# Kernel tuning notes

Measured on AMD Instinct MI355X. Metric: run time of the kernel, lower is better.

## Reference

```python
import jax, jax.numpy as jnp
import numpy as np

N_QUBITS = 6
N_LAYERS = 2
QSVT_DEGREE = 3
DT_RANK = max(N_QUBITS // 2, 1)
OUT_DIM = 3 * N_QUBITS
PI = np.float32(np.pi)
DT_MIN, DT_MAX = 1e-3, 0.1
BATCH, SEQ = 256, 512


def _ry_mat(theta):
    c = jnp.cos(theta / 2)
    s = jnp.sin(theta / 2)
    row0 = jnp.stack([c, -s], axis=-1)
    row1 = jnp.stack([s, c], axis=-1)
    return jnp.stack([row0, row1], axis=-2).astype(jnp.complex64)


def _rz_mat(theta):
    e = jnp.exp(-0.5j * theta.astype(jnp.complex64))
    z = jnp.zeros_like(e)
    row0 = jnp.stack([e, z], axis=-1)
    row1 = jnp.stack([z, jnp.conj(e)], axis=-1)
    return jnp.stack([row0, row1], axis=-2)


def _rx_mat(theta):
    c = jnp.cos(theta / 2).astype(jnp.complex64)
    s = jnp.sin(theta / 2).astype(jnp.complex64)
    row0 = jnp.stack([c, -1j * s], axis=-1)
    row1 = jnp.stack([-1j * s, c], axis=-1)
    return jnp.stack([row0, row1], axis=-2)


def _apply1(state, mat, w):
    # state: (B, 2, ..., 2) tensor over N_QUBITS axes; mat: (2,2) or batched (B,2,2)
    state = jnp.moveaxis(state, 1 + w, -1)
    if mat.ndim == 3:
        state = jnp.einsum('bij,b...j->b...i', mat, state)
    else:
        state = jnp.einsum('ij,b...j->b...i', mat, state)
    return jnp.moveaxis(state, -1, 1 + w)


def _cnot(state, c, t):
    state = jnp.moveaxis(state, (1 + c, 1 + t), (-2, -1))
    state = state.at[..., 1, :].set(state[..., 1, ::-1])
    return jnp.moveaxis(state, (-2, -1), (1 + c, 1 + t))


def _crx(state, theta, c, t):
    state = jnp.moveaxis(state, (1 + c, 1 + t), (-2, -1))
    m = _rx_mat(theta)
    state = state.at[..., 1, :].set(jnp.einsum('ij,...j->...i', m, state[..., 1, :]))
    return jnp.moveaxis(state, (-2, -1), (1 + c, 1 + t))


def _circuit(h, x, dt, circuit_params, poly_coeffs, qsvt_params):
    """Batched statevector simulation of the selective QSVT + unified ansatz qnode."""
    n = N_QUBITS
    B = h.shape[0]
    state = jnp.zeros((B,) + (2,) * n, jnp.complex64)
    state = state.at[(slice(None),) + (0,) * n].set(1.0 + 0.0j)
    # 1) state encoding RY(h[t-1])
    for i in range(n):
        state = _apply1(state, _ry_mat(h[:, i]), i)
    # 2) Delta-modulated QSVT: RZ rotations + bidirectional CNOT ring per degree
    qidx = 0
    n_qp = n * QSVT_DEGREE
    for deg in range(QSVT_DEGREE + 1):
        coeff = poly_coeffs[deg]
        for i in range(n):
            if qidx < n_qp:
                ang = coeff * dt[:, i] * qsvt_params[qidx] * PI
                qidx += 1
            else:
                ang = coeff * dt[:, i] * PI
            state = _apply1(state, _rz_mat(ang), i)
        for i in range(n - 1):
            state = _cnot(state, i, i + 1)
        state = _cnot(state, n - 1, 0)
        for i in range(n - 1, 0, -1):
            state = _cnot(state, i, i - 1)
    # 3) unified variational ansatz
    p = 0
    for _ in range(N_LAYERS):
        for i in range(n):
            state = _apply1(state, _rx_mat(circuit_params[p]), i)
            state = _apply1(state, _ry_mat(circuit_params[p + 1]), i)
            state = _apply1(state, _rz_mat(circuit_params[p + 2]), i)
            p += 3
        for i in range(n):
            state = _crx(state, circuit_params[p], i, (i + 1) % n)
            p += 1
        for i in range(n - 1, -1, -1):
            state = _crx(state, circuit_params[p], i, (i - 1) % n)
            p += 1
    # 4) Delta-modulated input RY(x * dt)
    for i in range(n):
        state = _apply1(state, _ry_mat(x[:, i] * dt[:, i]), i)
    # 5) Pauli X/Y/Z expectation values per qubit
    xs, ys, zs = [], [], []
    for i in range(n):
        s = jnp.moveaxis(state, 1 + i, 1).reshape(B, 2, -1)
        z = jnp.sum(jnp.conj(s[:, 0]) * s[:, 1], axis=-1)
        xs.append(2.0 * jnp.real(z))
        ys.append(2.0 * jnp.imag(z))
        zs.append(jnp.sum(jnp.abs(s[:, 0]) ** 2 - jnp.abs(s[:, 1]) ** 2, axis=-1))
    return jnp.stack(xs + ys + zs, axis=-1).astype(jnp.float32)  # (B, 3n)


def setup_inputs() -> dict:
    key = jax.random.key(0)
    ks = jax.random.split(key, 8)
    angles = jax.random.uniform(ks[0], (BATCH, SEQ, N_QUBITS), jnp.float32) * PI
    Wx = jax.random.normal(ks[1], (DT_RANK + 2 * N_QUBITS, N_QUBITS), jnp.float32) / np.float32(np.sqrt(N_QUBITS))
    Wdt = jax.random.normal(ks[2], (N_QUBITS, DT_RANK), jnp.float32) / np.float32(np.sqrt(DT_RANK))
    dt = jnp.exp(jax.random.uniform(ks[3], (N_QUBITS,), jnp.float32) * np.float32(np.log(DT_MAX) - np.log(DT_MIN)) + np.float32(np.log(DT_MIN)))
    bdt = dt + jnp.log(-jnp.expm1(-dt))
    poly_coeffs = jax.random.normal(ks[4], (QSVT_DEGREE + 1,), jnp.float32) * 0.1
    qsvt_params = jax.random.normal(ks[5], (N_QUBITS * QSVT_DEGREE,), jnp.float32) * 0.1
    circuit_params = jax.random.normal(ks[6], (5 * N_QUBITS * N_LAYERS,), jnp.float32) * 0.1
    D = jnp.ones((OUT_DIM,), jnp.float32)
    Wc = jax.random.normal(ks[7], (OUT_DIM, N_QUBITS), jnp.float32) / np.float32(np.sqrt(N_QUBITS))
    return {"angles": angles, "Wx": Wx, "Wdt": Wdt, "bdt": bdt, "poly_coeffs": poly_coeffs, "qsvt_params": qsvt_params, "circuit_params": circuit_params, "D": D, "Wc": Wc}


def reference(angles, Wx, Wdt, bdt, poly_coeffs, qsvt_params, circuit_params, D, Wc):
    x_dbc = angles @ Wx.T  # (B,S, dt_rank + 2n)
    dt_raw = x_dbc[..., :DT_RANK]
    # B slice computed in the original but never used in forward
    C = x_dbc[..., DT_RANK + N_QUBITS:]
    dt_angles = jnp.tanh(jax.nn.softplus(dt_raw @ Wdt.T + bdt)) * PI  # (B,S,n)
    # quantum part is detached in the original (detach().cpu() before the qnode)
    sg = jax.lax.stop_gradient
    xs = (jnp.moveaxis(sg(angles), 1, 0), jnp.moveaxis(sg(dt_angles), 1, 0))
    cp, pc, qp = sg(circuit_params), sg(poly_coeffs), sg(qsvt_params)
    h0 = jnp.zeros((angles.shape[0], N_QUBITS), jnp.float32)

    def step(h, xt):
        x_t, dt_t = xt
        meas = _circuit(h, x_t, dt_t, cp, pc, qp)
        return meas[:, 2 * N_QUBITS:], meas  # carry = PauliZ block

    _, meas = jax.lax.scan(step, h0, xs)
    h_full = jnp.moveaxis(meas, 0, 1)  # (B,S,3n)
    return (C @ Wc.T) * h_full + D * jnp.concatenate([angles] * 3, axis=-1)
```

## Files before the change

### kernel.cpp

```cpp
#include <hip/hip_runtime.h>
#include <math.h>

#define BATCH 256
#define SEQ 512
#define SDS 54
#define PI_F 3.14159265358979323846f

template<int CTRL>
__device__ __forceinline__ float fdpp(float v) {
    return __int_as_float(__builtin_amdgcn_mov_dpp(__float_as_int(v), CTRL, 0xF, 0xF, true));
}
template<int L>
__device__ __forceinline__ float rdl(float v) {
    return __int_as_float(__builtin_amdgcn_readlane(__float_as_int(v), L));
}
__device__ __forceinline__ float rdlv(float v, int l) {
    return __int_as_float(__builtin_amdgcn_readlane(__float_as_int(v), l));
}
template<int M>
__device__ __forceinline__ float shxm(float v) {
    if constexpr (M == 1)       return fdpp<0xB1>(v);
    else if constexpr (M == 2)  return fdpp<0x4E>(v);
    else if constexpr (M == 8)  return fdpp<0x128>(v);
    else if constexpr (M == 32) return __shfl_xor(v, 32, 64);
    else return __int_as_float(__builtin_amdgcn_ds_swizzle(__float_as_int(v), (M << 10) | 0x1F));
}
__device__ __forceinline__ float redsum64(float v) {
    v += fdpp<0x128>(v);
    v += fdpp<0x124>(v);
    v += fdpp<0x122>(v);
    v += fdpp<0x121>(v);
    return (rdl<0>(v) + rdl<16>(v)) + (rdl<32>(v) + rdl<48>(v));
}
__device__ __forceinline__ float xorf(float v, int m) {
    return __int_as_float(__float_as_int(v) ^ m);
}
__device__ __forceinline__ int permf(int x) {
    const int cs[11] = {0,1,2,3,4,5,5,4,3,2,1};
    const int ts[11] = {1,2,3,4,5,0,4,3,2,1,0};
#pragma unroll
    for (int k = 10; k >= 0; k--) {
        int cb = (x >> (5 - cs[k])) & 1;
        x ^= cb << (5 - ts[k]);
    }
    return x;
}
__device__ __forceinline__ void cmul4(const float* c,
    float vr, float vi, float ar, float ai, float br, float bi, float cr, float ci,
    float& nr, float& ni) {
    nr = c[0]*vr - c[1]*vi + c[2]*ar - c[3]*ai + c[4]*br - c[5]*bi + c[6]*cr - c[7]*ci;
    ni = c[0]*vi + c[1]*vr + c[2]*ai + c[3]*ar + c[4]*bi + c[5]*br + c[6]*ci + c[7]*cr;
}
__device__ __forceinline__ void ringapply(const float* rc,
    float vr, float vi, float br, float bi, float cr, float ci, float dr, float di,
    float& nr, float& ni) {
    nr = rc[0]*vr - rc[1]*bi - rc[2]*ci + rc[3]*dr;
    ni = rc[0]*vi + rc[1]*br + rc[2]*cr + rc[3]*di;
}

__global__ __launch_bounds__(256) void prep_kernel(
    const float* __restrict__ angles, const float* __restrict__ Wx,
    const float* __restrict__ Wdt, const float* __restrict__ bdt,
    const float* __restrict__ D, const float* __restrict__ Wc,
    float* __restrict__ sd)
{
    int gid = blockIdx.x * blockDim.x + threadIdx.x;
    if (gid >= BATCH * SEQ) return;
    const float* a = angles + (size_t)gid * 6;
    float ang[6];
#pragma unroll
    for (int i = 0; i < 6; i++) ang[i] = a[i];
    float dtr[3];
#pragma unroll
    for (int r = 0; r < 3; r++) {
        float s = 0.f;
#pragma unroll
        for (int k = 0; k < 6; k++) s += ang[k] * Wx[r * 6 + k];
        dtr[r] = s;
    }
    float* rec = sd + (size_t)gid * SDS;
    float dtv[6];
#pragma unroll
    for (int i = 0; i < 6; i++) {
        float x = bdt[i];
#pragma unroll
        for (int r = 0; r < 3; r++) x += dtr[r] * Wdt[i * 3 + r];
        float sp = (x > 15.f) ? x : log1pf(expf(x));
        dtv[i] = tanhf(sp) * PI_F;
        rec[i] = dtv[i];
        float th = ang[i] * dtv[i];
        rec[6 + i]  = cosf(th);
        rec[12 + i] = sinf(th);
    }
    float C[6];
#pragma unroll
    for (int i = 0; i < 6; i++) {
        float s = 0.f;
#pragma unroll
        for (int k = 0; k < 6; k++) s += ang[k] * Wx[(9 + i) * 6 + k];
        C[i] = s;
    }
#pragma unroll
    for (int j = 0; j < 18; j++) {
        float s = 0.f;
#pragma unroll
        for (int i = 0; i < 6; i++) s += C[i] * Wc[j * 6 + i];
        rec[18 + j] = s;
        rec[36 + j] = D[j] * ang[j % 6];
    }
}

__global__ __launch_bounds__(64) void umat_kernel(const float* __restrict__ cp,
                                                  float2* __restrict__ um)
{
    const int lane = threadIdx.x;
    const int col = blockIdx.x;
    int bitv[6];
#pragma unroll
    for (int i = 0; i < 6; i++) bitv[i] = (lane >> (5 - i)) & 1;

    float qc[2][3][8], rc[2][6][4];
#pragma unroll
    for (int l = 0; l < 2; l++) {
        float g00r[6], g00i[6], g01r[6], g01i[6], g10r[6], g10i[6], g11r[6], g11i[6];
#pragma unroll
        for (int i = 0; i < 6; i++) {
            float ax = cp[l * 30 + i * 3 + 0];
            float ay = cp[l * 30 + i * 3 + 1];
            float az = cp[l * 30 + i * 3 + 2];
            float ca = cosf(0.5f * ax), sa = sinf(0.5f * ax);
            float cb = cosf(0.5f * ay), sb = sinf(0.5f * ay);
            float cg = cosf(0.5f * az), sg = sinf(0.5f * az);
            float m00r = cb * ca, m00i =  sb * sa;
            float m01r = -sb * ca, m01i = -cb * sa;
            float m10r =  sb * ca, m10i = -cb * sa;
            float m11r =  cb * ca, m11i = -sb * sa;
            g00r[i] = cg * m00r + sg * m00i; g00i[i] = cg * m00i - sg * m00r;
            g01r[i] = cg * m01r + sg * m01i; g01i[i] = cg * m01i - sg * m01r;
            g10r[i] = cg * m10r - sg * m10i; g10i[i] = cg * m10i + sg * m10r;
            g11r[i] = cg * m11r - sg * m11i; g11i[i] = cg * m11i + sg * m11r;
        }
#pragma unroll
        for (int pp = 0; pp < 3; pp++) {
            int aq = 2 * pp, bq = 2 * pp + 1;
            float dar = bitv[aq] ? g11r[aq] : g00r[aq], dai = bitv[aq] ? g11i[aq] : g00i[aq];
            float oar = bitv[aq] ? g10r[aq] : g01r[aq], oai = bitv[aq] ? g10i[aq] : g01i[aq];
            float dbr = bitv[bq] ? g11r[bq] : g00r[bq], dbi = bitv[bq] ? g11i[bq] : g00i[bq];
            float obr = bitv[bq] ? g10r[bq] : g01r[bq], obi = bitv[bq] ? g10i[bq] : g01i[bq];
            qc[l][pp][0] = dar * dbr - dai * dbi;  qc[l][pp][1] = dar * dbi + dai * dbr;
            qc[l][pp][2] = oar * dbr - oai * dbi;  qc[l][pp][3] = oar * dbi + oai * dbr;
            qc[l][pp][4] = dar * obr - dai * obi;  qc[l][pp][5] = dar * obi + dai * obr;
            qc[l][pp][6] = oar * obr - oai * obi;  qc[l][pp][7] = oar * obi + oai * obr;
        }
        const int Aq[6] = {0, 2, 4, 5, 3, 1};
        const int Bq[6] = {1, 3, 5, 4, 2, 0};
#pragma unroll
        for (int o = 0; o < 6; o++) {
            float tha = (o < 3) ? cp[l * 30 + 18 + 2 * o]     : cp[l * 30 + 24 + 2 * (o - 3)];
            float thb = (o < 3) ? cp[l * 30 + 18 + 2 * o + 1] : cp[l * 30 + 24 + 2 * (o - 3) + 1];
            float ca = cosf(0.5f * tha), sa = sinf(0.5f * tha);
            float cb = cosf(0.5f * thb), sb = sinf(0.5f * thb);
            int ba = bitv[Aq[o]], bb = bitv[Bq[o]];
            float mx0 = ba ? ca : 1.f, sae = ba ? sa : 0.f;
            float ny0 = bb ? cb : 1.f, sbe = bb ? sb : 0.f;
            rc[l][o][0] = ny0 * mx0; rc[l][o][1] = -ny0 * sae;
            rc[l][o][2] = -mx0 * sbe; rc[l][o][3] = -sae * sbe;
        }
    }

    float re = (lane == col) ? 1.f : 0.f;
    float im = 0.f;
    auto p1q = [&](int mi, int mj, const float* c) {
        float ar = __shfl_xor(re, mi, 64), ai = __shfl_xor(im, mi, 64);
        float br = __shfl_xor(re, mj, 64), bi = __shfl_xor(im, mj, 64);
        float cr = __shfl_xor(re, mi | mj, 64), ci = __shfl_xor(im, mi | mj, 64);
        float nr, ni;
        cmul4(c, re, im, ar, ai, br, bi, cr, ci, nr, ni);
        re = nr; im = ni;
    };
    auto rng = [&](int mb, int mc, const float* c) {
        float br = __shfl_xor(re, mb, 64), bi = __shfl_xor(im, mb, 64);
        float cr = __shfl_xor(re, mc, 64), ci = __shfl_xor(im, mc, 64);
        float dr = __shfl_xor(re, mb | mc, 64), di = __shfl_xor(im, mb | mc, 64);
        float nr, ni;
        ringapply(c, re, im, br, bi, cr, ci, dr, di, nr, ni);
        re = nr; im = ni;
    };
#pragma unroll
    for (int l = 0; l < 2; l++) {
        p1q(32, 16, qc[l][0]);
        p1q(8, 4, qc[l][1]);
        p1q(2, 1, qc[l][2]);
        rng(16, 8, rc[l][0]);
        rng(4, 2, rc[l][1]);
        rng(1, 32, rc[l][2]);
        rng(2, 4, rc[l][3]);
        rng(8, 16, rc[l][4]);
        rng(32, 1, rc[l][5]);
    }
    um[(size_t)lane * 64 + col] = make_float2(re, im);
}

__global__ __launch_bounds__(256, 1) void step_kernel(
    const float* __restrict__ sd, const float* __restrict__ pc,
    const float* __restrict__ qp, const float2* __restrict__ um,
    float* __restrict__ out)
{
    __shared__ float2 sPart[4][64];
    __shared__ float sZX[12];
    __shared__ float sY[6];
    const int tid = threadIdx.x;
    const int wave = tid >> 6;
    const int lane = tid & 63;
    const int b = blockIdx.x;

    int bitv[6];
#pragma unroll
    for (int i = 0; i < 6; i++) bitv[i] = (lane >> (5 - i)) & 1;
    int sflip[6];
#pragma unroll
    for (int q = 0; q < 6; q++) sflip[q] = bitv[q] ? (int)0x80000000 : 0;

    const int jbase = wave * 16;
    float2 row[16];
#pragma unroll
    for (int jj = 0; jj < 16; jj++) row[jj] = um[(size_t)lane * 64 + jbase + jj];

    float A[6], sel[6];
    {
        int x1 = permf(lane), x2 = permf(x1), x3 = permf(x2), x4 = permf(x3);
#pragma unroll
        for (int i = 0; i < 6; i++) {
            float u0 = pc[0] * PI_F * qp[0 * 6 + i];
            float u1 = pc[1] * PI_F * qp[1 * 6 + i];
            float u2 = pc[2] * PI_F * qp[2 * 6 + i];
            float u3 = pc[3] * PI_F;
            float t1 = ((x1 >> (5 - i)) & 1) ? 0.5f : -0.5f;
            float t2 = ((x2 >> (5 - i)) & 1) ? 0.5f : -0.5f;
            float t3 = ((x3 >> (5 - i)) & 1) ? 0.5f : -0.5f;
            float t4 = ((x4 >> (5 - i)) & 1) ? 0.5f : -0.5f;
            A[i] = u3 * t1 + u2 * t2 + u1 * t3 + u0 * t4;
            sel[i] = (float)((x4 >> (5 - i)) & 1);
        }
    }

    const float* sdb = sd + (size_t)b * SEQ * SDS;
    float* outb = out + (size_t)b * SEQ * 18;

    float h0 = 0.f, h1 = 0.f, h2 = 0.f, h3 = 0.f, h4 = 0.f, h5 = 0.f;

    for (int t = 0; t < SEQ; t++) {
        const float* r = sdb + (size_t)t * SDS;
        float d0 = r[0], d1 = r[1], d2 = r[2], d3 = r[3], d4 = r[4], d5 = r[5];
        float ct[6], st[6];
#pragma unroll
        for (int q = 0; q < 6; q++) { ct[q] = r[6 + q]; st[q] = r[12 + q]; }

        float phi = A[0]*d0 + A[1]*d1 + A[2]*d2 + A[3]*d3 + A[4]*d4 + A[5]*d5;
        float sph, cph;
        __sincosf(phi, &sph, &cph);

        float ss0, cc0, ss1, cc1, ss2, cc2, ss3, cc3, ss4, cc4, ss5, cc5;
        __sincosf(0.5f * h0, &ss0, &cc0);
        __sincosf(0.5f * h1, &ss1, &cc1);
        __sincosf(0.5f * h2, &ss2, &cc2);
        __sincosf(0.5f * h3, &ss3, &cc3);
        __sincosf(0.5f * h4, &ss4, &cc4);
        __sincosf(0.5f * h5, &ss5, &cc5);
        float f0 = fmaf(sel[0], ss0 - cc0, cc0);
        float f1 = fmaf(sel[1], ss1 - cc1, cc1);
        float f2 = fmaf(sel[2], ss2 - cc2, cc2);
        float f3 = fmaf(sel[3], ss3 - cc3, cc3);
        float f4 = fmaf(sel[4], ss4 - cc4, cc4);
        float f5 = fmaf(sel[5], ss5 - cc5, cc5);
        float prod = ((f0 * f1) * (f2 * f3)) * (f4 * f5);
        float pr = prod * cph, pi = prod * sph;

        float ar0 = 0.f, ai0 = 0.f, ar1 = 0.f, ai1 = 0.f;
#pragma unroll
        for (int jj = 0; jj < 16; jj += 2) {
            float sr0 = rdlv(pr, jbase + jj);
            float si0 = rdlv(pi, jbase + jj);
            float sr1 = rdlv(pr, jbase + jj + 1);
            float si1 = rdlv(pi, jbase + jj + 1);
            ar0 = fmaf(row[jj].x, sr0, ar0);
            ar0 = fmaf(-row[jj].y, si0, ar0);
            ai0 = fmaf(row[jj].x, si0, ai0);
            ai0 = fmaf(row[jj].y, sr0, ai0);
            ar1 = fmaf(row[jj + 1].x, sr1, ar1);
            ar1 = fmaf(-row[jj + 1].y, si1, ar1);
            ai1 = fmaf(row[jj + 1].x, si1, ai1);
            ai1 = fmaf(row[jj + 1].y, sr1, ai1);
        }
        sPart[wave][lane] = make_float2(ar0 + ar1, ai0 + ai1);
        __syncthreads();
        float2 q0v = sPart[0][lane], q1v = sPart[1][lane];
        float2 q2v = sPart[2][lane], q3v = sPart[3][lane];
        float re = (q0v.x + q1v.x) + (q2v.x + q3v.x);
        float im = (q0v.y + q1v.y) + (q2v.y + q3v.y);

        if (wave == 0) {
            float p = re * re + im * im;
            float Z0 = redsum64(xorf(p, sflip[0]));
            float Z1 = redsum64(xorf(p, sflip[1]));
            float Z2 = redsum64(xorf(p, sflip[2]));
            float Z3 = redsum64(xorf(p, sflip[3]));
            float Z4 = redsum64(xorf(p, sflip[4]));
            float Z5 = redsum64(xorf(p, sflip[5]));
            if (lane == 0) {
                sZX[0] = Z0; sZX[1] = Z1; sZX[2] = Z2;
                sZX[3] = Z3; sZX[4] = Z4; sZX[5] = Z5;
            }
        } else if (wave == 1) {
            float g0r = shxm<32>(re), g0i = shxm<32>(im);
            float g1r = shxm<16>(re), g1i = shxm<16>(im);
            float g2r = shxm<8>(re),  g2i = shxm<8>(im);
            float X0 = redsum64(re * g0r + im * g0i);
            float X1 = redsum64(re * g1r + im * g1i);
            float X2 = redsum64(re * g2r + im * g2i);
            float Y0 = redsum64(xorf(re * g0i - im * g0r, sflip[0]));
            float Y1 = redsum64(xorf(re * g1i - im * g1r, sflip[1]));
            float Y2 = redsum64(xorf(re * g2i - im * g2r, sflip[2]));
            if (lane == 0) {
                sZX[6] = X0; sZX[7] = X1; sZX[8] = X2;
                sY[0] = Y0; sY[1] = Y1; sY[2] = Y2;
            }
        } else if (wave == 2) {
            float g3r = shxm<4>(re), g3i = shxm<4>(im);
            float g4r = shxm<2>(re), g4i = shxm<2>(im);
            float g5r = shxm<1>(re), g5i = shxm<1>(im);
            float X3 = redsum64(re * g3r + im * g3i);
            float X4 = redsum64(re * g4r + im * g4i);
            float X5 = redsum64(re * g5r + im * g5i);
            float Y3 = redsum64(xorf(re * g3i - im * g3r, sflip[3]));
            float Y4 = redsum64(xorf(re * g4i - im * g4r, sflip[4]));
            float Y5 = redsum64(xorf(re * g5i - im * g5r, sflip[5]));
            if (lane == 0) {
                sZX[9] = X3; sZX[10] = X4; sZX[11] = X5;
                sY[3] = Y3; sY[4] = Y4; sY[5] = Y5;
            }
        }
        __syncthreads();

        float Zv[6], Xv[6];
#pragma unroll
        for (int q = 0; q < 6; q++) { Zv[q] = sZX[q]; Xv[q] = sZX[6 + q]; }
        h0 = ct[0] * Zv[0] - st[0] * Xv[0];
        h1 = ct[1] * Zv[1] - st[1] * Xv[1];
        h2 = ct[2] * Zv[2] - st[2] * Xv[2];
        h3 = ct[3] * Zv[3] - st[3] * Xv[3];
        h4 = ct[4] * Zv[4] - st[4] * Xv[4];
        h5 = ct[5] * Zv[5] - st[5] * Xv[5];

        if (wave == 0 && lane == 0) {
            float* o = outb + (size_t)t * 18;
            float hh[6] = {h0, h1, h2, h3, h4, h5};
#pragma unroll
            for (int q = 0; q < 6; q++) o[12 + q] = fmaf(r[30 + q], hh[q], r[48 + q]);
        }
        if (wave == 3 && lane == 0) {
            float* o = outb + (size_t)t * 18;
#pragma unroll
            for (int q = 0; q < 6; q++) {
                float px = ct[q] * Xv[q] + st[q] * Zv[q];
                o[q]     = fmaf(r[18 + q], px, r[36 + q]);
                o[6 + q] = fmaf(r[24 + q], sY[q], r[42 + q]);
            }
        }
    }
}

extern "C" void kernel_launch(void* const* d_in, const int* in_sizes, int n_in,
                              void* d_out, int out_size, void* d_ws, size_t ws_size,
                              hipStream_t stream) {
    const float* angles = (const float*)d_in[0];
    const float* Wx     = (const float*)d_in[1];
    const float* Wdt    = (const float*)d_in[2];
    const float* bdt    = (const float*)d_in[3];
    const float* pc     = (const float*)d_in[4];
    const float* qp     = (const float*)d_in[5];
    const float* cp     = (const float*)d_in[6];
    const float* D      = (const float*)d_in[7];
    const float* Wc     = (const float*)d_in[8];
    float* sd  = (float*)d_ws;
    float2* um = (float2*)(sd + (size_t)BATCH * SEQ * SDS);
    float* out = (float*)d_out;

    umat_kernel<<<64, 64, 0, stream>>>(cp, um);
    prep_kernel<<<(BATCH * SEQ) / 256, 256, 0, stream>>>(angles, Wx, Wdt, bdt, D, Wc, sd);
    step_kernel<<<BATCH, 256, 0, stream>>>(sd, pc, qp, um, out);
}
```

Measured before the change: 728.2 us.

## Prefetch next step data, use lightweight LDS barriers, rebalance reductions across waves

Loads the next timestep's 18 per-step scalars into registers during the current step, so global-load latency is hidden behind the sequential recurrence. Replaces __syncthreads with an explicit LDS-only waitcnt plus s_barrier wrapped in sched barriers, so pending global loads are not drained at each barrier. It also spreads the X/Y reductions across three waves instead of two and packs Z/X/Y into one aligned shared array read as float4s. Costs are higher register pressure and a hand-coded waitcnt encoding that must be correct.

```diff
diff --git a/kernel.cpp b/kernel.cpp
--- a/kernel.cpp
+++ b/kernel.cpp
@@ -34,6 +34,12 @@
 }
 __device__ __forceinline__ float xorf(float v, int m) {
     return __int_as_float(__float_as_int(v) ^ m);
+}
+__device__ __forceinline__ void wg_barrier_lds() {
+    __builtin_amdgcn_sched_barrier(0);
+    __builtin_amdgcn_s_waitcnt(0xC07F);
+    __builtin_amdgcn_s_barrier();
+    __builtin_amdgcn_sched_barrier(0);
 }
 __device__ __forceinline__ int permf(int x) {
     const int cs[11] = {0,1,2,3,4,5,5,4,3,2,1};
@@ -207,8 +213,7 @@
     float* __restrict__ out)
 {
     __shared__ float2 sPart[4][64];
-    __shared__ float sZX[12];
-    __shared__ float sY[6];
+    __shared__ __align__(16) float sZXY[20];
     const int tid = threadIdx.x;
     const int wave = tid >> 6;
     const int lane = tid & 63;
@@ -249,14 +254,17 @@
 
     float h0 = 0.f, h1 = 0.f, h2 = 0.f, h3 = 0.f, h4 = 0.f, h5 = 0.f;
 
+    float cd[18], nd[18];
+#pragma unroll
+    for (int k = 0; k < 18; k++) cd[k] = sdb[k];
+
     for (int t = 0; t < SEQ; t++) {
-        const float* r = sdb + (size_t)t * SDS;
-        float d0 = r[0], d1 = r[1], d2 = r[2], d3 = r[3], d4 = r[4], d5 = r[5];
-        float ct[6], st[6];
-#pragma unroll
-        for (int q = 0; q < 6; q++) { ct[q] = r[6 + q]; st[q] = r[12 + q]; }
-
-        float phi = A[0]*d0 + A[1]*d1 + A[2]*d2 + A[3]*d3 + A[4]*d4 + A[5]*d5;
+        const float* r  = sdb + (size_t)t * SDS;
+        const float* rn = sdb + (size_t)((t + 1 < SEQ) ? t + 1 : t) * SDS;
+#pragma unroll
+        for (int k = 0; k < 18; k++) nd[k] = rn[k];
+
+        float phi = A[0]*cd[0] + A[1]*cd[1] + A[2]*cd[2] + A[3]*cd[3] + A[4]*cd[4] + A[5]*cd[5];
         float sph, cph;
         __sincosf(phi, &sph, &cph);
 
@@ -293,7 +301,7 @@
             ai1 = fmaf(row[jj + 1].y, sr1, ai1);
         }
         sPart[wave][lane] = make_float2(ar0 + ar1, ai0 + ai1);
-        __syncthreads();
+        wg_barrier_lds();
         float2 q0v = sPart[0][lane], q1v = sPart[1][lane];
         float2 q2v = sPart[2][lane], q3v = sPart[3][lane];
         float re = (q0v.x + q1v.x) + (q2v.x + q3v.x);
@@ -308,49 +316,47 @@
             float Z4 = redsum64(xorf(p, sflip[4]));
             float Z5 = redsum64(xorf(p, sflip[5]));
             if (lane == 0) {
-                sZX[0] = Z0; sZX[1] = Z1; sZX[2] = Z2;
-                sZX[3] = Z3; sZX[4] = Z4; sZX[5] = Z5;
+                sZXY[0] = Z0; sZXY[1] = Z1; sZXY[2] = Z2;
+                sZXY[3] = Z3; sZXY[4] = Z4; sZXY[5] = Z5;
             }
         } else if (wave == 1) {
             float g0r = shxm<32>(re), g0i = shxm<32>(im);
             float g1r = shxm<16>(re), g1i = shxm<16>(im);
-            float g2r = shxm<8>(re),  g2i = shxm<8>(im);
             float X0 = redsum64(re * g0r + im * g0i);
             float X1 = redsum64(re * g1r + im * g1i);
-            float X2 = redsum64(re * g2r + im * g2i);
             float Y0 = redsum64(xorf(re * g0i - im * g0r, sflip[0]));
             float Y1 = redsum64(xorf(re * g1i - im * g1r, sflip[1]));
+            if (lane == 0) { sZXY[6] = X0; sZXY[7] = X1; sZXY[12] = Y0; sZXY[13] = Y1; }
+        } else if (wave == 2) {
+            float g2r = shxm<8>(re), g2i = shxm<8>(im);
+            float g3r = shxm<4>(re), g3i = shxm<4>(im);
+            float X2 = redsum64(re * g2r + im * g2i);
+            float X3 = redsum64(re * g3r + im * g3i);
             float Y2 = redsum64(xorf(re * g2i - im * g2r, sflip[2]));
-            if (lane == 0) {
-                sZX[6] = X0; sZX[7] = X1; sZX[8] = X2;
-                sY[0] = Y0; sY[1] = Y1; sY[2] = Y2;
-            }
-        } else if (wave == 2) {
-            float g3r = shxm<4>(re), g3i = shxm<4>(im);
+            float Y3 = redsum64(xorf(re * g3i - im * g3r, sflip[3]));
+            if (lane == 0) { sZXY[8] = X2; sZXY[9] = X3; sZXY[14] = Y2; sZXY[15] = Y3; }
+        } else {
             float g4r = shxm<2>(re), g4i = shxm<2>(im);
             float g5r = shxm<1>(re), g5i = shxm<1>(im);
-            float X3 = redsum64(re * g3r + im * g3i);
             float X4 = redsum64(re * g4r + im * g4i);
             float X5 = redsum64(re * g5r + im * g5i);
-            float Y3 = redsum64(xorf(re * g3i - im * g3r, sflip[3]));
             float Y4 = redsum64(xorf(re * g4i - im * g4r, sflip[4]));
             float Y5 = redsum64(xorf(re * g5i - im * g5r, sflip[5]));
-            if (lane == 0) {
-                sZX[9] = X3; sZX[10] = X4; sZX[11] = X5;
-                sY[3] = Y3; sY[4] = Y4; sY[5] = Y5;
-            }
-        }
-        __syncthreads();
-
-        float Zv[6], Xv[6];
-#pragma unroll
-        for (int q = 0; q < 6; q++) { Zv[q] = sZX[q]; Xv[q] = sZX[6 + q]; }
-        h0 = ct[0] * Zv[0] - st[0] * Xv[0];
-        h1 = ct[1] * Zv[1] - st[1] * Xv[1];
-        h2 = ct[2] * Zv[2] - st[2] * Xv[2];
-        h3 = ct[3] * Zv[3] - st[3] * Xv[3];
-        h4 = ct[4] * Zv[4] - st[4] * Xv[4];
-        h5 = ct[5] * Zv[5] - st[5] * Xv[5];
+            if (lane == 0) { sZXY[10] = X4; sZXY[11] = X5; sZXY[16] = Y4; sZXY[17] = Y5; }
+        }
+        wg_barrier_lds();
+
+        float4 v0 = ((const float4*)sZXY)[0];
+        float4 v1 = ((const float4*)sZXY)[1];
+        float4 v2 = ((const float4*)sZXY)[2];
+        float Zv[6] = {v0.x, v0.y, v0.z, v0.w, v1.x, v1.y};
+        float Xv[6] = {v1.z, v1.w, v2.x, v2.y, v2.z, v2.w};
+        h0 = cd[6]  * Zv[0] - cd[12] * Xv[0];
+        h1 = cd[7]  * Zv[1] - cd[13] * Xv[1];
+        h2 = cd[8]  * Zv[2] - cd[14] * Xv[2];
+        h3 = cd[9]  * Zv[3] - cd[15] * Xv[3];
+        h4 = cd[10] * Zv[4] - cd[16] * Xv[4];
+        h5 = cd[11] * Zv[5] - cd[17] * Xv[5];
 
         if (wave == 0 && lane == 0) {
             float* o = outb + (size_t)t * 18;
@@ -362,11 +368,14 @@
             float* o = outb + (size_t)t * 18;
 #pragma unroll
             for (int q = 0; q < 6; q++) {
-                float px = ct[q] * Xv[q] + st[q] * Zv[q];
+                float px = cd[6 + q] * Xv[q] + cd[12 + q] * Zv[q];
                 o[q]     = fmaf(r[18 + q], px, r[36 + q]);
-                o[6 + q] = fmaf(r[24 + q], sY[q], r[42 + q]);
+                o[6 + q] = fmaf(r[24 + q], sZXY[12 + q], r[42 + q]);
             }
         }
+
+#pragma unroll
+        for (int k = 0; k < 18; k++) cd[k] = nd[k];
     }
 }
 
```

After: 712.8 us. 1.02x faster.
